# Kernel tuning notes

Hardware: AMD Instinct MI355X
Metric: run time of the kernel (lower is better)

The kernel has to match this reference:

```python
import jax, jax.numpy as jnp
import numpy as np

B, L, D_MODEL = 2, 4096, 256
D_STATE, D_CONV, EXPAND = 16, 4, 2
D_INNER = EXPAND * D_MODEL
DT_RANK = D_MODEL // 16
D_FF = 2048


def setup_inputs() -> dict:
    key = jax.random.key(0)
    ks = jax.random.split(key, 14)
    s = 0.02
    A_log = jnp.log(jnp.tile(jnp.arange(1, D_STATE + 1, dtype=jnp.float32), (D_INNER, 1)))
    return {
        "x": jax.random.normal(ks[0], (B, L, D_MODEL), jnp.float32),
        "in_proj_w": jax.random.normal(ks[1], (2 * D_INNER, D_MODEL), jnp.float32) * s,
        "conv_w": jax.random.normal(ks[2], (D_INNER, D_CONV), jnp.float32) * s,
        "conv_b": jax.random.normal(ks[3], (D_INNER,), jnp.float32) * s,
        "x_proj_w": jax.random.normal(ks[4], (DT_RANK + 2 * D_STATE, D_INNER), jnp.float32) * s,
        "dt_proj_w": jax.random.normal(ks[5], (D_INNER, DT_RANK), jnp.float32) * s,
        "dt_proj_b": jax.random.uniform(ks[6], (D_INNER,), jnp.float32, -4.0, -2.0),
        "A_log": A_log,
        "D": jnp.ones((D_INNER,), jnp.float32),
        "out_proj_w": jax.random.normal(ks[7], (D_MODEL, D_INNER), jnp.float32) * s,
        "lin1_w": jax.random.normal(ks[8], (D_FF, D_MODEL), jnp.float32) * s,
        "lin1_b": jnp.zeros((D_FF,), jnp.float32),
        "lin2_w": jax.random.normal(ks[9], (D_FF, D_FF), jnp.float32) * s,
        "lin2_b": jnp.zeros((D_FF,), jnp.float32),
    }


def reference(x, in_proj_w, conv_w, conv_b, x_proj_w, dt_proj_w, dt_proj_b,
              A_log, D, out_proj_w, lin1_w, lin1_b, lin2_w, lin2_b):
    b, l, _ = x.shape
    d_inner = conv_w.shape[0]
    d_state = A_log.shape[1]
    dt_rank = dt_proj_w.shape[1]
    d_conv = conv_w.shape[1]

    # in_proj -> split into x and gate z
    xz = x @ in_proj_w.T                       # (B,L,2*Din)
    xin, z = jnp.split(xz, 2, axis=-1)

    # causal depthwise conv1d + SiLU
    xc = jnp.transpose(xin, (0, 2, 1))         # (B,Din,L)
    xc = jax.lax.conv_general_dilated(
        xc, conv_w[:, None, :], (1,), [(d_conv - 1, 0)],
        dimension_numbers=("NCH", "OIH", "NCH"), feature_group_count=d_inner)
    xc = xc + conv_b[None, :, None]
    u = jax.nn.silu(jnp.transpose(xc, (0, 2, 1)))  # (B,L,Din)

    # input-dependent SSM params
    x_dbl = u @ x_proj_w.T                     # (B,L,dt_rank+2*N)
    dt, Bt, Ct = jnp.split(x_dbl, [dt_rank, dt_rank + d_state], axis=-1)
    delta = jax.nn.softplus(dt @ dt_proj_w.T + dt_proj_b)  # (B,L,Din)

    A = -jnp.exp(A_log)                        # (Din,N)
    dA = jnp.exp(delta[..., None] * A)         # (B,L,Din,N)
    dBu = delta[..., None] * Bt[:, :, None, :] * u[..., None]  # (B,L,Din,N)

    def step(h, inp):
        dA_t, dBu_t, C_t = inp
        h = dA_t * h + dBu_t                   # (B,Din,N)
        y = jnp.einsum("bdn,bn->bd", h, C_t)
        return h, y

    h0 = jnp.zeros((b, d_inner, d_state), x.dtype)
    _, ys = jax.lax.scan(step, h0, (jnp.swapaxes(dA, 0, 1),
                                    jnp.swapaxes(dBu, 0, 1),
                                    jnp.swapaxes(Ct, 0, 1)))
    y = jnp.swapaxes(ys, 0, 1) + u * D         # (B,L,Din)
    y = y * jax.nn.silu(z)
    m = y @ out_proj_w.T                       # (B,L,d_model)

    # trailing MLP: lin2(relu(lin1(.)))
    h1 = jax.nn.relu(m @ lin1_w.T + lin1_b)
    return h1 @ lin2_w.T + lin2_b
```

## Files before the change

kernel.cpp:

```cpp
#include <hip/hip_runtime.h>
#include <hip/hip_bf16.h>
#include <stdint.h>

#define BB  2
#define LL  4096
#define DM  256
#define DI  512
#define NST 16
#define DTR 16
#define DFF 2048
#define ML  (BB*LL)

#define NCHUNK 128
#define CHUNK  32
#define BDN    (BB*DI*NST)

typedef __attribute__((ext_vector_type(8))) short s16x8;
typedef __attribute__((ext_vector_type(4))) float f32x4;

__device__ __forceinline__ ushort f2bf(float f) {
  union { float f; uint32_t u; } v; v.f = f;
  return (ushort)((v.u + 0x7FFFu + ((v.u >> 16) & 1u)) >> 16);
}

__device__ __forceinline__ void async16(const void* g, void* l) {
  __builtin_amdgcn_global_load_lds(
      (const __attribute__((address_space(1))) void*)g,
      (__attribute__((address_space(3))) void*)l, 16, 0, 0);
}

__global__ void k_f2b(const float* __restrict__ src, ushort* __restrict__ dst, int n4) {
  int i = blockIdx.x * 256 + threadIdx.x;
  if (i >= n4) return;
  f32x4 v = ((const f32x4*)src)[i];
  *(ushort4*)&dst[i * 4] = make_ushort4(f2bf(v[0]), f2bf(v[1]), f2bf(v[2]), f2bf(v[3]));
}

__global__ void k_xprojw(const float* __restrict__ src, ushort* __restrict__ dst) {
  int i = blockIdx.x * 256 + threadIdx.x;
  if (i >= 128 * DI / 4) return;
  int e = i * 4;
  int r = e >> 9;
  int c = e & 511;
  ushort4 o;
  if (r < DTR + 2 * NST) {
    f32x4 v = *(const f32x4*)&src[r * DI + c];
    o = make_ushort4(f2bf(v[0]), f2bf(v[1]), f2bf(v[2]), f2bf(v[3]));
  } else {
    o = make_ushort4(0, 0, 0, 0);
  }
  *(ushort4*)&dst[e] = o;
}

template<int OUTF, int OUTB, int BIAS, int RELU>
__global__ __launch_bounds__(256)
void k_gemm(const ushort* __restrict__ A, const ushort* __restrict__ W,
            const float* __restrict__ bias,
            float* __restrict__ outF, ushort* __restrict__ outB,
            int M, int N, int K) {
  __shared__ __align__(16) ushort As[128 * 32];
  __shared__ __align__(16) ushort Bs[128 * 32];
  const int tid  = threadIdx.x;
  const int lane = tid & 63;
  const int wv   = tid >> 6;
  const int m0 = blockIdx.y << 7;
  const int n0 = blockIdx.x << 7;
  const int wr = (wv >> 1) << 6;
  const int wc = (wv & 1) << 6;
  const int lr = lane & 15;
  const int hi = lane >> 4;

  f32x4 acc[4][4] = {};

  const int sr0 = (wv << 5) + (lane >> 2);
  const int sc  = lane & 3;

  for (int k0 = 0; k0 < K; k0 += 32) {
#pragma unroll
    for (int j = 0; j < 2; ++j) {
      const int r  = sr0 + j * 16;
      const int cs = sc ^ (r & 3);
      async16(A + (size_t)(m0 + r) * K + k0 + cs * 8, &As[((wv << 5) + j * 16) * 32]);
      async16(W + (size_t)(n0 + r) * K + k0 + cs * 8, &Bs[((wv << 5) + j * 16) * 32]);
    }
    __syncthreads();

    s16x8 af[4], bf_[4];
#pragma unroll
    for (int mi = 0; mi < 4; ++mi) {
      const int row = wr + mi * 16 + lr;
      af[mi] = *(const s16x8*)&As[row * 32 + ((hi ^ (row & 3)) << 3)];
    }
#pragma unroll
    for (int ni = 0; ni < 4; ++ni) {
      const int row = wc + ni * 16 + lr;
      bf_[ni] = *(const s16x8*)&Bs[row * 32 + ((hi ^ (row & 3)) << 3)];
    }
#pragma unroll
    for (int mi = 0; mi < 4; ++mi)
#pragma unroll
      for (int ni = 0; ni < 4; ++ni)
        acc[mi][ni] = __builtin_amdgcn_mfma_f32_16x16x32_bf16(af[mi], bf_[ni], acc[mi][ni], 0, 0, 0);
    __syncthreads();
  }

#pragma unroll
  for (int mi = 0; mi < 4; ++mi) {
#pragma unroll
    for (int ni = 0; ni < 4; ++ni) {
      const int gc = n0 + wc + ni * 16 + lr;
      const float b = BIAS ? bias[gc] : 0.f;
#pragma unroll
      for (int i = 0; i < 4; ++i) {
        const int gr = m0 + wr + mi * 16 + (hi << 2) + i;
        float v = acc[mi][ni][i] + b;
        if (RELU) v = fmaxf(v, 0.f);
        if (OUTF) outF[(size_t)gr * N + gc] = v;
        if (OUTB) outB[(size_t)gr * N + gc] = f2bf(v);
      }
    }
  }
}

__global__ void k_conv(const float* __restrict__ xz, const float* __restrict__ cw,
                       const float* __restrict__ cb,
                       float* __restrict__ u, ushort* __restrict__ u_bf) {
  const int i = blockIdx.x * 256 + threadIdx.x;
  if (i >= ML * DI / 4) return;
  const int d4 = i & (DI / 4 - 1);
  const int bl = i / (DI / 4);
  const int l  = bl & (LL - 1);
  const int d  = d4 << 2;
  f32x4 acc;
  acc[0] = cb[d]; acc[1] = cb[d + 1]; acc[2] = cb[d + 2]; acc[3] = cb[d + 3];
#pragma unroll
  for (int j = 0; j < 4; ++j) {
    const int lj = l - 3 + j;
    if (lj >= 0) {
      const f32x4 xv = *(const f32x4*)&xz[(size_t)(bl + j - 3) * 1024 + d];
      acc[0] += xv[0] * cw[(d + 0) * 4 + j];
      acc[1] += xv[1] * cw[(d + 1) * 4 + j];
      acc[2] += xv[2] * cw[(d + 2) * 4 + j];
      acc[3] += xv[3] * cw[(d + 3) * 4 + j];
    }
  }
  f32x4 o;
#pragma unroll
  for (int c = 0; c < 4; ++c) o[c] = acc[c] / (1.f + __expf(-acc[c]));
  *(f32x4*)&u[(size_t)bl * DI + d] = o;
  *(ushort4*)&u_bf[(size_t)bl * DI + d] =
      make_ushort4(f2bf(o[0]), f2bf(o[1]), f2bf(o[2]), f2bf(o[3]));
}

__global__ void k_dtproj(const float* __restrict__ xdbl, const float* __restrict__ w,
                         const float* __restrict__ bias, float* __restrict__ delta) {
  const int m = blockIdx.x;
  const int tid = threadIdx.x;
  __shared__ float sdt[16];
  if (tid < 16) sdt[tid] = xdbl[(size_t)m * 128 + tid];
  __syncthreads();
#pragma unroll
  for (int rep = 0; rep < 2; ++rep) {
    const int nn = tid + rep * 256;
    float acc = bias[nn];
#pragma unroll
    for (int k = 0; k < 16; ++k) acc += sdt[k] * w[nn * 16 + k];
    delta[(size_t)m * DI + nn] = (acc > 15.f) ? acc : log1pf(__expf(acc));
  }
}

__global__ __launch_bounds__(256)
void k_scan1(const float* __restrict__ delta, const float* __restrict__ u,
             const float* __restrict__ xdbl, const float* __restrict__ A_log,
             float* __restrict__ Pw, float* __restrict__ Sw) {
  const int c = blockIdx.x;
  const int b = blockIdx.y >> 1;
  const int d = ((blockIdx.y & 1) << 8) + threadIdx.x;
  __shared__ float sB[CHUNK][16];
  {
    const int i = threadIdx.x * 2;
    const int t = i >> 4, n = i & 15;
    const size_t g = ((size_t)b * LL + (size_t)c * CHUNK + t) * 128 + DTR + n;
    *(float2*)&sB[t][n] = *(const float2*)&xdbl[g];
  }
  float An[16];
#pragma unroll
  for (int j = 0; j < 4; ++j) {
    f32x4 a = *(const f32x4*)&A_log[d * 16 + j * 4];
#pragma unroll
    for (int q = 0; q < 4; ++q) An[j * 4 + q] = -__expf(a[q]);
  }
  float P[16], S[16];
#pragma unroll
  for (int n = 0; n < 16; ++n) { P[n] = 1.f; S[n] = 0.f; }
  __syncthreads();

  const size_t rowbase = ((size_t)b * LL + (size_t)c * CHUNK) * DI + d;
  float dt = delta[rowbase];
  float ut = u[rowbase];
  for (int t = 0; t < CHUNK; ++t) {
    float dt_n = 0.f, ut_n = 0.f;
    if (t + 1 < CHUNK) {
      dt_n = delta[rowbase + (size_t)(t + 1) * DI];
      ut_n = u[rowbase + (size_t)(t + 1) * DI];
    }
    const float k = dt * ut;
#pragma unroll
    for (int n = 0; n < 16; ++n) {
      const float dA = __expf(dt * An[n]);
      S[n] = fmaf(dA, S[n], k * sB[t][n]);
      P[n] *= dA;
    }
    dt = dt_n; ut = ut_n;
  }
  float* Pp = Pw + ((size_t)c * BDN) + ((size_t)b * DI + d) * 16;
  float* Sp = Sw + ((size_t)c * BDN) + ((size_t)b * DI + d) * 16;
#pragma unroll
  for (int j = 0; j < 4; ++j) {
    f32x4 pv, sv;
#pragma unroll
    for (int q = 0; q < 4; ++q) { pv[q] = P[j * 4 + q]; sv[q] = S[j * 4 + q]; }
    *(f32x4*)&Pp[j * 4] = pv;
    *(f32x4*)&Sp[j * 4] = sv;
  }
}

__global__ void k_scan2(float* __restrict__ Pw, const float* __restrict__ Sw) {
  const int f = blockIdx.x * 256 + threadIdx.x;
  float h = 0.f;
#pragma unroll 4
  for (int c = 0; c < NCHUNK; ++c) {
    const float Pc = Pw[(size_t)c * BDN + f];
    const float Sc = Sw[(size_t)c * BDN + f];
    Pw[(size_t)c * BDN + f] = h;
    h = fmaf(Pc, h, Sc);
  }
}

__global__ __launch_bounds__(256)
void k_scan3(const float* __restrict__ delta, const float* __restrict__ u,
             const float* __restrict__ xdbl, const float* __restrict__ xz,
             const float* __restrict__ A_log, const float* __restrict__ Dp,
             const float* __restrict__ Hs, ushort* __restrict__ y_bf) {
  const int c = blockIdx.x;
  const int b = blockIdx.y >> 1;
  const int d = ((blockIdx.y & 1) << 8) + threadIdx.x;
  __shared__ float sB[CHUNK][16], sC[CHUNK][16];
  {
    const int i = threadIdx.x * 2;
    const int t = i >> 4, n = i & 15;
    const size_t g = ((size_t)b * LL + (size_t)c * CHUNK + t) * 128 + DTR + n;
    *(float2*)&sB[t][n] = *(const float2*)&xdbl[g];
    *(float2*)&sC[t][n] = *(const float2*)&xdbl[g + NST];
  }
  float An[16];
#pragma unroll
  for (int j = 0; j < 4; ++j) {
    f32x4 a = *(const f32x4*)&A_log[d * 16 + j * 4];
#pragma unroll
    for (int q = 0; q < 4; ++q) An[j * 4 + q] = -__expf(a[q]);
  }
  float h[16];
  {
    const float* Hp = Hs + ((size_t)c * BDN) + ((size_t)b * DI + d) * 16;
#pragma unroll
    for (int j = 0; j < 4; ++j) {
      f32x4 v = *(const f32x4*)&Hp[j * 4];
#pragma unroll
      for (int q = 0; q < 4; ++q) h[j * 4 + q] = v[q];
    }
  }
  const float Dd = Dp[d];
  __syncthreads();

  const size_t rowbase = ((size_t)b * LL + (size_t)c * CHUNK) * DI + d;
  const size_t zbase   = ((size_t)b * LL + (size_t)c * CHUNK) * 1024 + DI + d;
  float dt = delta[rowbase];
  float ut = u[rowbase];
  float zt = xz[zbase];
  for (int t = 0; t < CHUNK; ++t) {
    float dt_n = 0.f, ut_n = 0.f, zt_n = 0.f;
    if (t + 1 < CHUNK) {
      dt_n = delta[rowbase + (size_t)(t + 1) * DI];
      ut_n = u[rowbase + (size_t)(t + 1) * DI];
      zt_n = xz[zbase + (size_t)(t + 1) * 1024];
    }
    const float k = dt * ut;
    float y = 0.f;
#pragma unroll
    for (int n = 0; n < 16; ++n) {
      const float dA = __expf(dt * An[n]);
      h[n] = fmaf(dA, h[n], k * sB[t][n]);
      y = fmaf(h[n], sC[t][n], y);
    }
    y = (y + ut * Dd) * (zt / (1.f + __expf(-zt)));
    y_bf[rowbase + (size_t)t * DI] = f2bf(y);
    dt = dt_n; ut = ut_n; zt = zt_n;
  }
}

extern "C" void kernel_launch(void* const* d_in, const int* in_sizes, int n_in,
                              void* d_out, int out_size, void* d_ws, size_t ws_size,
                              hipStream_t stream) {
  const float* x          = (const float*)d_in[0];
  const float* in_proj_w  = (const float*)d_in[1];
  const float* conv_w     = (const float*)d_in[2];
  const float* conv_b     = (const float*)d_in[3];
  const float* x_proj_w   = (const float*)d_in[4];
  const float* dt_proj_w  = (const float*)d_in[5];
  const float* dt_proj_b  = (const float*)d_in[6];
  const float* A_log      = (const float*)d_in[7];
  const float* Dp         = (const float*)d_in[8];
  const float* out_proj_w = (const float*)d_in[9];
  const float* lin1_w     = (const float*)d_in[10];
  const float* lin1_b     = (const float*)d_in[11];
  const float* lin2_w     = (const float*)d_in[12];
  const float* lin2_b     = (const float*)d_in[13];
  float* out = (float*)d_out;

  char* p = (char*)d_ws;
  auto carve = [&](size_t bytes) -> char* {
    char* r = p;
    p += (bytes + 255) & ~(size_t)255;
    return r;
  };
  ushort* x_bf   = (ushort*)carve((size_t)ML * DM * 2);
  ushort* wip_bf = (ushort*)carve((size_t)2 * DI * DM * 2);
  float*  xz     = (float*) carve((size_t)ML * 1024 * 4);
  float*  u      = (float*) carve((size_t)ML * DI * 4);
  ushort* u_bf   = (ushort*)carve((size_t)ML * DI * 2);
  ushort* xpw_bf = (ushort*)carve((size_t)128 * DI * 2);
  float*  xdbl   = (float*) carve((size_t)ML * 128 * 4);
  float*  delta  = (float*) carve((size_t)ML * DI * 4);
  ushort* y_bf   = (ushort*)carve((size_t)ML * DI * 2);
  ushort* opw_bf = (ushort*)carve((size_t)DM * DI * 2);
  float*  Pws    = (float*) carve((size_t)NCHUNK * BDN * 4);
  float*  Sws    = (float*) carve((size_t)NCHUNK * BDN * 4);
  ushort* m_bf   = u_bf;
  ushort* h1_bf  = (ushort*)xz;
  ushort* l1w_bf = (ushort*)delta;
  ushort* l2w_bf = (ushort*)u;

  k_f2b<<<(ML * DM / 4 + 255) / 256, 256, 0, stream>>>(x, x_bf, ML * DM / 4);
  k_f2b<<<(2 * DI * DM / 4 + 255) / 256, 256, 0, stream>>>(in_proj_w, wip_bf, 2 * DI * DM / 4);
  k_gemm<1, 0, 0, 0><<<dim3(1024 / 128, ML / 128), 256, 0, stream>>>(
      x_bf, wip_bf, nullptr, xz, nullptr, ML, 1024, DM);
  k_conv<<<(ML * DI / 4 + 255) / 256, 256, 0, stream>>>(xz, conv_w, conv_b, u, u_bf);
  k_xprojw<<<(128 * DI / 4 + 255) / 256, 256, 0, stream>>>(x_proj_w, xpw_bf);
  k_gemm<1, 0, 0, 0><<<dim3(1, ML / 128), 256, 0, stream>>>(
      u_bf, xpw_bf, nullptr, xdbl, nullptr, ML, 128, DI);
  k_dtproj<<<ML, 256, 0, stream>>>(xdbl, dt_proj_w, dt_proj_b, delta);
  k_scan1<<<dim3(NCHUNK, BB * 2), 256, 0, stream>>>(delta, u, xdbl, A_log, Pws, Sws);
  k_scan2<<<BDN / 256, 256, 0, stream>>>(Pws, Sws);
  k_scan3<<<dim3(NCHUNK, BB * 2), 256, 0, stream>>>(delta, u, xdbl, xz, A_log, Dp,
                                                    Pws, y_bf);
  k_f2b<<<(DM * DI / 4 + 255) / 256, 256, 0, stream>>>(out_proj_w, opw_bf, DM * DI / 4);
  k_gemm<0, 1, 0, 0><<<dim3(DM / 128, ML / 128), 256, 0, stream>>>(
      y_bf, opw_bf, nullptr, nullptr, m_bf, ML, DM, DI);
  k_f2b<<<(DFF * DM / 4 + 255) / 256, 256, 0, stream>>>(lin1_w, l1w_bf, DFF * DM / 4);
  k_gemm<0, 1, 1, 1><<<dim3(DFF / 128, ML / 128), 256, 0, stream>>>(
      m_bf, l1w_bf, lin1_b, nullptr, h1_bf, ML, DFF, DM);
  k_f2b<<<(DFF * DFF / 4 + 255) / 256, 256, 0, stream>>>(lin2_w, l2w_bf, DFF * DFF / 4);
  k_gemm<1, 0, 1, 0><<<dim3(DFF / 128, ML / 128), 256, 0, stream>>>(
      h1_bf, l2w_bf, lin2_b, out, nullptr, ML, DFF, DFF);
}
```

Before: 393.1 us.

## Triple-buffer GEMM with async prefetch and XCD swizzle; fuse dt_proj into scans

The GEMM now keeps three LDS stages with two K-tiles prefetched ahead, waits on vmcnt instead of doing two __syncthreads per tile, and raises wave priority around the MFMA block. It also remaps workgroups across 8 XCDs, changes the LDS XOR swizzle to use (row>>1)&3, and computes dt_proj plus softplus inside both scan kernels, so the delta buffer and the k_dtproj launch go away. This targets GEMM memory latency and the delta write/read traffic. In exchange the scans redo the 16-term dot product and softplus, the swizzle assumes the grid size divides by 8, and the vmcnt(4) count is tied to the number of async loads per stage.

```diff
diff --git a/kernel.cpp b/kernel.cpp
--- a/kernel.cpp
+++ b/kernel.cpp
@@ -58,13 +58,19 @@
             const float* __restrict__ bias,
             float* __restrict__ outF, ushort* __restrict__ outB,
             int M, int N, int K) {
-  __shared__ __align__(16) ushort As[128 * 32];
-  __shared__ __align__(16) ushort Bs[128 * 32];
+  __shared__ __align__(16) ushort AsB[3][128 * 32];
+  __shared__ __align__(16) ushort BsB[3][128 * 32];
   const int tid  = threadIdx.x;
   const int lane = tid & 63;
   const int wv   = tid >> 6;
-  const int m0 = blockIdx.y << 7;
-  const int n0 = blockIdx.x << 7;
+
+  const int nwg  = gridDim.x * gridDim.y;
+  const int flat = blockIdx.y * gridDim.x + blockIdx.x;
+  const int cpx  = nwg >> 3;
+  const int swz  = (flat & 7) * cpx + (flat >> 3);
+  const int m0 = (swz / gridDim.x) << 7;
+  const int n0 = (swz % gridDim.x) << 7;
+
   const int wr = (wv >> 1) << 6;
   const int wc = (wv & 1) << 6;
   const int lr = lane & 15;
@@ -75,33 +81,59 @@
   const int sr0 = (wv << 5) + (lane >> 2);
   const int sc  = lane & 3;
 
-  for (int k0 = 0; k0 < K; k0 += 32) {
+  const int nt = K >> 5;
+
+  auto STAGE = [&](int t, int bi) {
+    const int k0 = t << 5;
 #pragma unroll
     for (int j = 0; j < 2; ++j) {
       const int r  = sr0 + j * 16;
-      const int cs = sc ^ (r & 3);
-      async16(A + (size_t)(m0 + r) * K + k0 + cs * 8, &As[((wv << 5) + j * 16) * 32]);
-      async16(W + (size_t)(n0 + r) * K + k0 + cs * 8, &Bs[((wv << 5) + j * 16) * 32]);
-    }
-    __syncthreads();
-
+      const int cs = sc ^ ((r >> 1) & 3);
+      async16(A + (size_t)(m0 + r) * K + k0 + cs * 8, &AsB[bi][((wv << 5) + j * 16) * 32]);
+      async16(W + (size_t)(n0 + r) * K + k0 + cs * 8, &BsB[bi][((wv << 5) + j * 16) * 32]);
+    }
+  };
+
+  STAGE(0, 0);
+  STAGE(1, 1);
+
+  int cur = 0;
+  for (int t = 0; t < nt; ++t) {
+    if (t + 1 < nt) { asm volatile("s_waitcnt vmcnt(4)" ::: "memory"); }
+    else            { asm volatile("s_waitcnt vmcnt(0)" ::: "memory"); }
+    __builtin_amdgcn_s_barrier();
+    __builtin_amdgcn_sched_barrier(0);
+
+    if (t + 2 < nt) {
+      int nx2 = cur + 2; if (nx2 >= 3) nx2 -= 3;
+      STAGE(t + 2, nx2);
+    }
+
+    const ushort* As = AsB[cur];
+    const ushort* Bs = BsB[cur];
     s16x8 af[4], bf_[4];
 #pragma unroll
     for (int mi = 0; mi < 4; ++mi) {
       const int row = wr + mi * 16 + lr;
-      af[mi] = *(const s16x8*)&As[row * 32 + ((hi ^ (row & 3)) << 3)];
+      af[mi] = *(const s16x8*)&As[row * 32 + ((hi ^ ((row >> 1) & 3)) << 3)];
     }
 #pragma unroll
     for (int ni = 0; ni < 4; ++ni) {
       const int row = wc + ni * 16 + lr;
-      bf_[ni] = *(const s16x8*)&Bs[row * 32 + ((hi ^ (row & 3)) << 3)];
-    }
+      bf_[ni] = *(const s16x8*)&Bs[row * 32 + ((hi ^ ((row >> 1) & 3)) << 3)];
+    }
+    asm volatile("s_waitcnt lgkmcnt(0)" ::: "memory");
+    __builtin_amdgcn_sched_barrier(0);
+
+    __builtin_amdgcn_s_setprio(1);
 #pragma unroll
     for (int mi = 0; mi < 4; ++mi)
 #pragma unroll
       for (int ni = 0; ni < 4; ++ni)
         acc[mi][ni] = __builtin_amdgcn_mfma_f32_16x16x32_bf16(af[mi], bf_[ni], acc[mi][ni], 0, 0, 0);
-    __syncthreads();
+    __builtin_amdgcn_s_setprio(0);
+
+    cur = (cur + 1 == 3) ? 0 : cur + 1;
   }
 
 #pragma unroll
@@ -152,58 +184,44 @@
       make_ushort4(f2bf(o[0]), f2bf(o[1]), f2bf(o[2]), f2bf(o[3]));
 }
 
-__global__ void k_dtproj(const float* __restrict__ xdbl, const float* __restrict__ w,
-                         const float* __restrict__ bias, float* __restrict__ delta) {
-  const int m = blockIdx.x;
-  const int tid = threadIdx.x;
-  __shared__ float sdt[16];
-  if (tid < 16) sdt[tid] = xdbl[(size_t)m * 128 + tid];
-  __syncthreads();
-#pragma unroll
-  for (int rep = 0; rep < 2; ++rep) {
-    const int nn = tid + rep * 256;
-    float acc = bias[nn];
-#pragma unroll
-    for (int k = 0; k < 16; ++k) acc += sdt[k] * w[nn * 16 + k];
-    delta[(size_t)m * DI + nn] = (acc > 15.f) ? acc : log1pf(__expf(acc));
-  }
-}
-
 __global__ __launch_bounds__(256)
-void k_scan1(const float* __restrict__ delta, const float* __restrict__ u,
-             const float* __restrict__ xdbl, const float* __restrict__ A_log,
+void k_scan1(const float* __restrict__ u, const float* __restrict__ xdbl,
+             const float* __restrict__ A_log, const float* __restrict__ dtw,
+             const float* __restrict__ dtb,
              float* __restrict__ Pw, float* __restrict__ Sw) {
   const int c = blockIdx.x;
   const int b = blockIdx.y >> 1;
   const int d = ((blockIdx.y & 1) << 8) + threadIdx.x;
-  __shared__ float sB[CHUNK][16];
+  __shared__ float sdt[CHUNK][16], sB[CHUNK][16];
   {
     const int i = threadIdx.x * 2;
     const int t = i >> 4, n = i & 15;
-    const size_t g = ((size_t)b * LL + (size_t)c * CHUNK + t) * 128 + DTR + n;
-    *(float2*)&sB[t][n] = *(const float2*)&xdbl[g];
-  }
-  float An[16];
+    const size_t g = ((size_t)b * LL + (size_t)c * CHUNK + t) * 128 + n;
+    *(float2*)&sdt[t][n] = *(const float2*)&xdbl[g];
+    *(float2*)&sB[t][n]  = *(const float2*)&xdbl[g + DTR];
+  }
+  float An[16], wreg[16];
 #pragma unroll
   for (int j = 0; j < 4; ++j) {
     f32x4 a = *(const f32x4*)&A_log[d * 16 + j * 4];
-#pragma unroll
-    for (int q = 0; q < 4; ++q) An[j * 4 + q] = -__expf(a[q]);
-  }
+    f32x4 w = *(const f32x4*)&dtw[d * 16 + j * 4];
+#pragma unroll
+    for (int q = 0; q < 4; ++q) { An[j * 4 + q] = -__expf(a[q]); wreg[j * 4 + q] = w[q]; }
+  }
+  const float bd = dtb[d];
   float P[16], S[16];
 #pragma unroll
   for (int n = 0; n < 16; ++n) { P[n] = 1.f; S[n] = 0.f; }
   __syncthreads();
 
   const size_t rowbase = ((size_t)b * LL + (size_t)c * CHUNK) * DI + d;
-  float dt = delta[rowbase];
   float ut = u[rowbase];
   for (int t = 0; t < CHUNK; ++t) {
-    float dt_n = 0.f, ut_n = 0.f;
-    if (t + 1 < CHUNK) {
-      dt_n = delta[rowbase + (size_t)(t + 1) * DI];
-      ut_n = u[rowbase + (size_t)(t + 1) * DI];
-    }
+    const float ut_n = (t + 1 < CHUNK) ? u[rowbase + (size_t)(t + 1) * DI] : 0.f;
+    float a = bd;
+#pragma unroll
+    for (int k2 = 0; k2 < 16; ++k2) a = fmaf(sdt[t][k2], wreg[k2], a);
+    const float dt = (a > 15.f) ? a : log1pf(__expf(a));
     const float k = dt * ut;
 #pragma unroll
     for (int n = 0; n < 16; ++n) {
@@ -211,7 +229,7 @@
       S[n] = fmaf(dA, S[n], k * sB[t][n]);
       P[n] *= dA;
     }
-    dt = dt_n; ut = ut_n;
+    ut = ut_n;
   }
   float* Pp = Pw + ((size_t)c * BDN) + ((size_t)b * DI + d) * 16;
   float* Sp = Sw + ((size_t)c * BDN) + ((size_t)b * DI + d) * 16;
@@ -238,28 +256,32 @@
 }
 
 __global__ __launch_bounds__(256)
-void k_scan3(const float* __restrict__ delta, const float* __restrict__ u,
-             const float* __restrict__ xdbl, const float* __restrict__ xz,
-             const float* __restrict__ A_log, const float* __restrict__ Dp,
+void k_scan3(const float* __restrict__ u, const float* __restrict__ xdbl,
+             const float* __restrict__ xz, const float* __restrict__ A_log,
+             const float* __restrict__ dtw, const float* __restrict__ dtb,
+             const float* __restrict__ Dp,
              const float* __restrict__ Hs, ushort* __restrict__ y_bf) {
   const int c = blockIdx.x;
   const int b = blockIdx.y >> 1;
   const int d = ((blockIdx.y & 1) << 8) + threadIdx.x;
-  __shared__ float sB[CHUNK][16], sC[CHUNK][16];
+  __shared__ float sdt[CHUNK][16], sB[CHUNK][16], sC[CHUNK][16];
   {
     const int i = threadIdx.x * 2;
     const int t = i >> 4, n = i & 15;
-    const size_t g = ((size_t)b * LL + (size_t)c * CHUNK + t) * 128 + DTR + n;
-    *(float2*)&sB[t][n] = *(const float2*)&xdbl[g];
-    *(float2*)&sC[t][n] = *(const float2*)&xdbl[g + NST];
-  }
-  float An[16];
+    const size_t g = ((size_t)b * LL + (size_t)c * CHUNK + t) * 128 + n;
+    *(float2*)&sdt[t][n] = *(const float2*)&xdbl[g];
+    *(float2*)&sB[t][n]  = *(const float2*)&xdbl[g + DTR];
+    *(float2*)&sC[t][n]  = *(const float2*)&xdbl[g + DTR + NST];
+  }
+  float An[16], wreg[16];
 #pragma unroll
   for (int j = 0; j < 4; ++j) {
     f32x4 a = *(const f32x4*)&A_log[d * 16 + j * 4];
-#pragma unroll
-    for (int q = 0; q < 4; ++q) An[j * 4 + q] = -__expf(a[q]);
-  }
+    f32x4 w = *(const f32x4*)&dtw[d * 16 + j * 4];
+#pragma unroll
+    for (int q = 0; q < 4; ++q) { An[j * 4 + q] = -__expf(a[q]); wreg[j * 4 + q] = w[q]; }
+  }
+  const float bd = dtb[d];
   float h[16];
   {
     const float* Hp = Hs + ((size_t)c * BDN) + ((size_t)b * DI + d) * 16;
@@ -275,16 +297,18 @@
 
   const size_t rowbase = ((size_t)b * LL + (size_t)c * CHUNK) * DI + d;
   const size_t zbase   = ((size_t)b * LL + (size_t)c * CHUNK) * 1024 + DI + d;
-  float dt = delta[rowbase];
   float ut = u[rowbase];
   float zt = xz[zbase];
   for (int t = 0; t < CHUNK; ++t) {
-    float dt_n = 0.f, ut_n = 0.f, zt_n = 0.f;
+    float ut_n = 0.f, zt_n = 0.f;
     if (t + 1 < CHUNK) {
-      dt_n = delta[rowbase + (size_t)(t + 1) * DI];
       ut_n = u[rowbase + (size_t)(t + 1) * DI];
       zt_n = xz[zbase + (size_t)(t + 1) * 1024];
     }
+    float a = bd;
+#pragma unroll
+    for (int k2 = 0; k2 < 16; ++k2) a = fmaf(sdt[t][k2], wreg[k2], a);
+    const float dt = (a > 15.f) ? a : log1pf(__expf(a));
     const float k = dt * ut;
     float y = 0.f;
 #pragma unroll
@@ -295,7 +319,7 @@
     }
     y = (y + ut * Dd) * (zt / (1.f + __expf(-zt)));
     y_bf[rowbase + (size_t)t * DI] = f2bf(y);
-    dt = dt_n; ut = ut_n; zt = zt_n;
+    ut = ut_n; zt = zt_n;
   }
 }
 
@@ -331,14 +355,13 @@
   ushort* u_bf   = (ushort*)carve((size_t)ML * DI * 2);
   ushort* xpw_bf = (ushort*)carve((size_t)128 * DI * 2);
   float*  xdbl   = (float*) carve((size_t)ML * 128 * 4);
-  float*  delta  = (float*) carve((size_t)ML * DI * 4);
   ushort* y_bf   = (ushort*)carve((size_t)ML * DI * 2);
   ushort* opw_bf = (ushort*)carve((size_t)DM * DI * 2);
+  ushort* l1w_bf = (ushort*)carve((size_t)DFF * DM * 2);
   float*  Pws    = (float*) carve((size_t)NCHUNK * BDN * 4);
   float*  Sws    = (float*) carve((size_t)NCHUNK * BDN * 4);
   ushort* m_bf   = u_bf;
   ushort* h1_bf  = (ushort*)xz;
-  ushort* l1w_bf = (ushort*)delta;
   ushort* l2w_bf = (ushort*)u;
 
   k_f2b<<<(ML * DM / 4 + 255) / 256, 256, 0, stream>>>(x, x_bf, ML * DM / 4);
@@ -349,11 +372,11 @@
   k_xprojw<<<(128 * DI / 4 + 255) / 256, 256, 0, stream>>>(x_proj_w, xpw_bf);
   k_gemm<1, 0, 0, 0><<<dim3(1, ML / 128), 256, 0, stream>>>(
       u_bf, xpw_bf, nullptr, xdbl, nullptr, ML, 128, DI);
-  k_dtproj<<<ML, 256, 0, stream>>>(xdbl, dt_proj_w, dt_proj_b, delta);
-  k_scan1<<<dim3(NCHUNK, BB * 2), 256, 0, stream>>>(delta, u, xdbl, A_log, Pws, Sws);
+  k_scan1<<<dim3(NCHUNK, BB * 2), 256, 0, stream>>>(u, xdbl, A_log, dt_proj_w,
+                                                    dt_proj_b, Pws, Sws);
   k_scan2<<<BDN / 256, 256, 0, stream>>>(Pws, Sws);
-  k_scan3<<<dim3(NCHUNK, BB * 2), 256, 0, stream>>>(delta, u, xdbl, xz, A_log, Dp,
-                                                    Pws, y_bf);
+  k_scan3<<<dim3(NCHUNK, BB * 2), 256, 0, stream>>>(u, xdbl, xz, A_log, dt_proj_w,
+                                                    dt_proj_b, Dp, Pws, y_bf);
   k_f2b<<<(DM * DI / 4 + 255) / 256, 256, 0, stream>>>(out_proj_w, opw_bf, DM * DI / 4);
   k_gemm<0, 1, 0, 0><<<dim3(DM / 128, ML / 128), 256, 0, stream>>>(
       y_bf, opw_bf, nullptr, nullptr, m_bf, ML, DM, DI);
```

After: 378.3 us. -3.8%, faster.
